# Optimization experiments

Hardware: AMD Instinct MI355X
Metric: run time of the kernel (lower is better)

Reference implementation:

```python
import jax, jax.numpy as jnp
import numpy as np

N_NODES = 100000
N_EDGES = 1600000
IN_DIM, HID_DIM, OUT_DIM = 32, 16, 8


def setup_inputs() -> dict:
    key = jax.random.key(0)
    ks = jax.random.split(key, 10)
    x = jax.random.normal(ks[0], (N_NODES, IN_DIM), dtype=jnp.float32)
    edge_index = jax.random.randint(ks[1], (2, N_EDGES), 0, N_NODES, dtype=jnp.int32)
    s1 = 1.0 / np.sqrt(IN_DIM)
    s2 = 1.0 / np.sqrt(HID_DIM)
    s3 = 1.0 / np.sqrt(OUT_DIM)
    return {
        "x": x,
        "edge_index": edge_index,
        # SAGEConv layer 1: lin_l (neighbor, with bias) and lin_r (root)
        "Wl1": jax.random.uniform(ks[2], (HID_DIM, IN_DIM), jnp.float32, -s1, s1),
        "bl1": jnp.zeros((HID_DIM,), jnp.float32),
        "Wr1": jax.random.uniform(ks[3], (HID_DIM, IN_DIM), jnp.float32, -s1, s1),
        # SAGEConv layer 2
        "Wl2": jax.random.uniform(ks[4], (OUT_DIM, HID_DIM), jnp.float32, -s2, s2),
        "bl2": jnp.zeros((OUT_DIM,), jnp.float32),
        "Wr2": jax.random.uniform(ks[5], (OUT_DIM, HID_DIM), jnp.float32, -s2, s2),
        # final Linear head
        "Wfc": jax.random.uniform(ks[6], (1, OUT_DIM), jnp.float32, -s3, s3),
        "bfc": jax.random.uniform(ks[7], (1,), jnp.float32, -s3, s3),
    }


def _sage_conv(x, src, dst, Wl, bl, Wr):
    # mean-aggregate neighbor messages x[src] at destination nodes
    msg_sum = jax.ops.segment_sum(x[src], dst, num_segments=N_NODES)  # [N, d]
    deg = jax.ops.segment_sum(jnp.ones((src.shape[0],), x.dtype), dst, num_segments=N_NODES)
    mean = msg_sum / jnp.maximum(deg, 1.0)[:, None]
    # out = lin_l(mean_neighbors) + lin_r(x_root)
    return mean @ Wl.T + bl + x @ Wr.T


def reference(x, edge_index, Wl1, bl1, Wr1, Wl2, bl2, Wr2, Wfc, bfc):
    src, dst = edge_index[0], edge_index[1]
    h = _sage_conv(x, src, dst, Wl1, bl1, Wr1)
    h = jax.nn.relu(h)
    h = _sage_conv(h, src, dst, Wl2, bl2, Wr2)
    return h @ Wfc.T + bfc  # [N, 1]
```

## Files before the change

### kernel.cpp

```cpp
#include <hip/hip_runtime.h>

#define NN 100000
#define NE 1600000
#define IN_DIM 32
#define HID_DIM 16
#define OUT_DIM 8

#define NPB 128
#define NBK ((NN + NPB - 1) / NPB)
#define CAP 3200
#define EPB 4096
#define EPT (EPB / 256)
#define NT_BUCKET ((NE + EPB - 1) / EPB)
#define NT_PRE1 ((NN + 255) / 256)
#define GRID1 (NT_BUCKET + NT_PRE1)
#define BF_STRIDE 16
#define SCAN_CHUNKS ((NBK + 255) / 256)

__global__ __launch_bounds__(256) void k_phase1(
    const float* __restrict__ x, const int* __restrict__ src, const int* __restrict__ dst,
    const float* __restrict__ Wl1, const float* __restrict__ bl1, const float* __restrict__ Wr1,
    const float* __restrict__ Wl2, const float* __restrict__ bl2, const float* __restrict__ Wr2,
    const float* __restrict__ Wfc, const float* __restrict__ bfc,
    int* __restrict__ bucketfill, unsigned int* __restrict__ bucket,
    float* __restrict__ z, float* __restrict__ rb, float* __restrict__ uvc)
{
    __shared__ int lcnt[NBK];
    __shared__ int lpos[NBK];
    __shared__ int lbase[NBK];
    __shared__ int lfill[NBK];
    __shared__ int sscan[256];
    __shared__ unsigned int ssorted[EPB];
    __shared__ unsigned short sbin[EPB];
    int tid = threadIdx.x;

    if (blockIdx.x < NT_BUCKET) {
        int e0 = blockIdx.x * EPB;
        int e1 = min(e0 + EPB, NE);
        int total = e1 - e0;

        for (int i = tid; i < NBK; i += 256) lcnt[i] = 0;
        __syncthreads();

        int myd[EPT];
#pragma unroll
        for (int k = 0; k < EPT; k++) {
            int e = e0 + k * 256 + tid;
            myd[k] = (e < e1) ? dst[e] : -1;
            if (myd[k] >= 0) atomicAdd(&lcnt[myd[k] >> 7], 1);
        }
        __syncthreads();

        int carry = 0;
        for (int ch = 0; ch < SCAN_CHUNKS; ch++) {
            int idx = ch * 256 + tid;
            int v = (idx < NBK) ? lcnt[idx] : 0;
            sscan[tid] = v;
            __syncthreads();
            for (int off = 1; off < 256; off <<= 1) {
                int t2 = (tid >= off) ? sscan[tid - off] : 0;
                __syncthreads();
                sscan[tid] += t2;
                __syncthreads();
            }
            if (idx < NBK) lpos[idx] = carry + sscan[tid] - v;
            carry += sscan[255];
            __syncthreads();
        }

        for (int i = tid; i < NBK; i += 256) {
            lbase[i] = (lcnt[i] > 0) ? atomicAdd(&bucketfill[i * BF_STRIDE], lcnt[i]) : 0;
            lfill[i] = lpos[i];
        }
        __syncthreads();

#pragma unroll
        for (int k = 0; k < EPT; k++) {
            if (myd[k] >= 0) {
                int e = e0 + k * 256 + tid;
                int s = src[e];
                int b = myd[k] >> 7;
                int p = atomicAdd(&lfill[b], 1);
                ssorted[p] = (unsigned)(myd[k] & (NPB - 1)) | ((unsigned)s << 7);
                sbin[p] = (unsigned short)b;
            }
        }
        __syncthreads();

        for (int i = tid; i < total; i += 256) {
            int b = sbin[i];
            bucket[(size_t)b * CAP + lbase[b] + (i - lpos[b])] = ssorted[i];
        }
    } else {
        int chunk = blockIdx.x - NT_BUCKET;
        float* sWl = (float*)ssorted;
        float* sWr = sWl + 512;
        float* sb  = (float*)sbin;
        for (int i = tid; i < HID_DIM * IN_DIM; i += 256) {
            sWl[i] = Wl1[i];
            sWr[i] = Wr1[i];
        }
        if (tid < HID_DIM) sb[tid] = bl1[tid];
        if (chunk == 0) {
            if (tid < HID_DIM) {
                float uu = 0.f, vv = 0.f;
#pragma unroll
                for (int o = 0; o < OUT_DIM; o++) {
                    uu += Wfc[o] * Wl2[o * HID_DIM + tid];
                    vv += Wfc[o] * Wr2[o * HID_DIM + tid];
                }
                uvc[tid] = uu;
                uvc[HID_DIM + tid] = vv;
            }
            if (tid == 0) {
                float c0 = bfc[0];
#pragma unroll
                for (int o = 0; o < OUT_DIM; o++) c0 += Wfc[o] * bl2[o];
                uvc[2 * HID_DIM] = c0;
            }
        }
        __syncthreads();
        int n = chunk * 256 + tid;
        if (n < NN) {
            float xv[IN_DIM];
            const float4* x4 = (const float4*)(x + (size_t)n * IN_DIM);
#pragma unroll
            for (int c = 0; c < 8; c++) {
                float4 b = x4[c];
                xv[c * 4 + 0] = b.x; xv[c * 4 + 1] = b.y;
                xv[c * 4 + 2] = b.z; xv[c * 4 + 3] = b.w;
            }
            float zo[HID_DIM], ro[HID_DIM];
#pragma unroll
            for (int o = 0; o < HID_DIM; o++) {
                float az = 0.f, ar = sb[o];
#pragma unroll
                for (int i = 0; i < IN_DIM; i++) {
                    az += sWl[o * IN_DIM + i] * xv[i];
                    ar += sWr[o * IN_DIM + i] * xv[i];
                }
                zo[o] = az; ro[o] = ar;
            }
            float4* z4 = (float4*)(z + (size_t)n * HID_DIM);
            float4* r4 = (float4*)(rb + (size_t)n * HID_DIM);
#pragma unroll
            for (int c = 0; c < 4; c++) {
                z4[c] = make_float4(zo[c*4], zo[c*4+1], zo[c*4+2], zo[c*4+3]);
                r4[c] = make_float4(ro[c*4], ro[c*4+1], ro[c*4+2], ro[c*4+3]);
            }
        }
    }
}

__global__ __launch_bounds__(256) void k_sort_gather(
    const int* __restrict__ bucketfill, const unsigned int* __restrict__ bucket,
    const float* __restrict__ z, const float* __restrict__ rb, const float* __restrict__ uvc,
    int* __restrict__ deg, int* __restrict__ rowstart, int* __restrict__ srcs,
    float* __restrict__ sv, float* __restrict__ tv)
{
    __shared__ int lcnt[NPB];
    __shared__ int lscan[NPB];
    __shared__ int lfill[NPB];
    __shared__ int lred[256];
    __shared__ int ssrc[CAP];

    int b = blockIdx.x;
    int tid = threadIdx.x;

    int part = 0;
    for (int i = tid; i < b; i += 256) part += bucketfill[i * BF_STRIDE];
    lred[tid] = part;
    __syncthreads();
    for (int off = 128; off > 0; off >>= 1) {
        if (tid < off) lred[tid] += lred[tid + off];
        __syncthreads();
    }
    int base = lred[0];
    int cntb = bucketfill[b * BF_STRIDE];
    const unsigned int* bk = bucket + (size_t)b * CAP;

    if (tid < NPB) lcnt[tid] = 0;
    __syncthreads();
    for (int i = tid; i < cntb; i += 256) atomicAdd(&lcnt[bk[i] & (NPB - 1)], 1);
    __syncthreads();
    if (tid < NPB) lscan[tid] = lcnt[tid];
    __syncthreads();
    for (int off = 1; off < NPB; off <<= 1) {
        int tvv = (tid >= off && tid < NPB) ? lscan[tid - off] : 0;
        __syncthreads();
        if (tid < NPB) lscan[tid] += tvv;
        __syncthreads();
    }
    if (tid < NPB) {
        int excl = lscan[tid] - lcnt[tid];
        lfill[tid] = excl;
        int node = b * NPB + tid;
        if (node < NN) { deg[node] = lcnt[tid]; rowstart[node] = base + excl; }
    }
    __syncthreads();
    for (int i = tid; i < cntb; i += 256) {
        unsigned v = bk[i];
        int d = v & (NPB - 1);
        int p = atomicAdd(&lfill[d], 1);
        int s = (int)(v >> 7);
        ssrc[p] = s;
        srcs[base + p] = s;
    }
    __syncthreads();

    int c = tid & 3;
    int nl0 = tid >> 2;
    float4 u4 = ((const float4*)uvc)[c];
    float4 v4 = ((const float4*)uvc)[4 + c];
#pragma unroll
    for (int pass = 0; pass < 2; pass++) {
        int nl = pass * 64 + nl0;
        int n2 = b * NPB + nl;
        if (n2 < NN) {
            int dg = lcnt[nl];
            int st = lscan[nl] - dg;
            float4 acc = {0.f, 0.f, 0.f, 0.f};
            for (int i = 0; i < dg; i++) {
                int sc = ssrc[st + i];
                float4 vz = ((const float4*)z)[sc * 4 + c];
                acc.x += vz.x; acc.y += vz.y; acc.z += vz.z; acc.w += vz.w;
            }
            float inv = 1.0f / fmaxf((float)dg, 1.0f);
            float4 r = ((const float4*)rb)[n2 * 4 + c];
            float h0 = fmaxf(acc.x * inv + r.x, 0.f);
            float h1 = fmaxf(acc.y * inv + r.y, 0.f);
            float h2 = fmaxf(acc.z * inv + r.z, 0.f);
            float h3 = fmaxf(acc.w * inv + r.w, 0.f);
            float ps = u4.x * h0 + u4.y * h1 + u4.z * h2 + u4.w * h3;
            float pt = v4.x * h0 + v4.y * h1 + v4.z * h2 + v4.w * h3;
            ps += __shfl_xor(ps, 1);
            ps += __shfl_xor(ps, 2);
            pt += __shfl_xor(pt, 1);
            pt += __shfl_xor(pt, 2);
            if (c == 0) { sv[n2] = ps; tv[n2] = pt; }
        }
    }
}

__global__ __launch_bounds__(256) void k_final(
    const int* __restrict__ srcs, const int* __restrict__ deg, const int* __restrict__ rowstart,
    const float* __restrict__ sv, const float* __restrict__ tv,
    const float* __restrict__ uvc, float* __restrict__ out)
{
    int v = blockIdx.x * 256 + threadIdx.x;
    if (v >= NN * 4) return;
    int n = v >> 2;
    int c = v & 3;
    int dg = deg[n];
    int st = rowstart[n];
    float acc = 0.f;
    for (int i = c; i < dg; i += 4) acc += sv[srcs[st + i]];
    acc += __shfl_xor(acc, 1);
    acc += __shfl_xor(acc, 2);
    if (c == 0) out[n] = acc / fmaxf((float)dg, 1.0f) + tv[n] + uvc[2 * HID_DIM];
}

extern "C" void kernel_launch(void* const* d_in, const int* in_sizes, int n_in,
                              void* d_out, int out_size, void* d_ws, size_t ws_size,
                              hipStream_t stream) {
    const float* x   = (const float*)d_in[0];
    const int*   ei  = (const int*)d_in[1];
    const float* Wl1 = (const float*)d_in[2];
    const float* bl1 = (const float*)d_in[3];
    const float* Wr1 = (const float*)d_in[4];
    const float* Wl2 = (const float*)d_in[5];
    const float* bl2 = (const float*)d_in[6];
    const float* Wr2 = (const float*)d_in[7];
    const float* Wfc = (const float*)d_in[8];
    const float* bfc = (const float*)d_in[9];
    float* out = (float*)d_out;

    const int* src = ei;
    const int* dst = ei + NE;

    int* bucketfill = (int*)d_ws;
    int* deg        = bucketfill + 12544;
    int* rowstart   = deg + NN;
    int* srcs       = rowstart + NN;
    float* uvc      = (float*)(srcs + NE);
    float* sv       = uvc + 40;
    float* tv       = sv + NN;
    unsigned int* bucket = (unsigned int*)(tv + NN);
    float* z        = (float*)(bucket + (size_t)NBK * CAP);
    float* rb       = z + (size_t)NN * HID_DIM;

    hipMemsetAsync(bucketfill, 0, NBK * BF_STRIDE * sizeof(int), stream);

    k_phase1<<<GRID1, 256, 0, stream>>>(x, src, dst, Wl1, bl1, Wr1,
                                        Wl2, bl2, Wr2, Wfc, bfc,
                                        bucketfill, bucket, z, rb, uvc);
    k_sort_gather<<<NBK, 256, 0, stream>>>(bucketfill, bucket, z, rb, uvc,
                                           deg, rowstart, srcs, sv, tv);
    k_final<<<((NN * 4) + 255) / 256, 256, 0, stream>>>(srcs, deg, rowstart, sv, tv, uvc, out);
}
```

Baseline: 164.5 us.

## Drop global CSR arrays; final pass re-reads buckets with LDS atomics

The sort-gather kernel no longer computes a global prefix over bucket fills or writes rowstart and the sorted source array (1.6M ints) to global memory. The final kernel now runs one block per bucket, re-reads the packed bucket entries and accumulates sv[src] into per-node shared-memory sums with LDS atomics. The layer-1 gather loop is also unrolled by four to keep more independent z loads in flight. This trades the CSR write and read traffic and the per-block serial prefix sum for a second bucket read and shared-memory float atomic contention. Float summation order also changes slightly.

```diff
diff --git a/kernel.cpp b/kernel.cpp
--- a/kernel.cpp
+++ b/kernel.cpp
@@ -155,27 +155,15 @@
 __global__ __launch_bounds__(256) void k_sort_gather(
     const int* __restrict__ bucketfill, const unsigned int* __restrict__ bucket,
     const float* __restrict__ z, const float* __restrict__ rb, const float* __restrict__ uvc,
-    int* __restrict__ deg, int* __restrict__ rowstart, int* __restrict__ srcs,
-    float* __restrict__ sv, float* __restrict__ tv)
+    int* __restrict__ deg, float* __restrict__ sv, float* __restrict__ tv)
 {
     __shared__ int lcnt[NPB];
     __shared__ int lscan[NPB];
     __shared__ int lfill[NPB];
-    __shared__ int lred[256];
     __shared__ int ssrc[CAP];
 
     int b = blockIdx.x;
     int tid = threadIdx.x;
-
-    int part = 0;
-    for (int i = tid; i < b; i += 256) part += bucketfill[i * BF_STRIDE];
-    lred[tid] = part;
-    __syncthreads();
-    for (int off = 128; off > 0; off >>= 1) {
-        if (tid < off) lred[tid] += lred[tid + off];
-        __syncthreads();
-    }
-    int base = lred[0];
     int cntb = bucketfill[b * BF_STRIDE];
     const unsigned int* bk = bucket + (size_t)b * CAP;
 
@@ -192,19 +180,16 @@
         __syncthreads();
     }
     if (tid < NPB) {
-        int excl = lscan[tid] - lcnt[tid];
-        lfill[tid] = excl;
+        lfill[tid] = lscan[tid] - lcnt[tid];
         int node = b * NPB + tid;
-        if (node < NN) { deg[node] = lcnt[tid]; rowstart[node] = base + excl; }
+        if (node < NN) deg[node] = lcnt[tid];
     }
     __syncthreads();
     for (int i = tid; i < cntb; i += 256) {
         unsigned v = bk[i];
         int d = v & (NPB - 1);
         int p = atomicAdd(&lfill[d], 1);
-        int s = (int)(v >> 7);
-        ssrc[p] = s;
-        srcs[base + p] = s;
+        ssrc[p] = (int)(v >> 7);
     }
     __syncthreads();
 
@@ -212,6 +197,7 @@
     int nl0 = tid >> 2;
     float4 u4 = ((const float4*)uvc)[c];
     float4 v4 = ((const float4*)uvc)[4 + c];
+    const float4* z4p = (const float4*)z;
 #pragma unroll
     for (int pass = 0; pass < 2; pass++) {
         int nl = pass * 64 + nl0;
@@ -220,9 +206,23 @@
             int dg = lcnt[nl];
             int st = lscan[nl] - dg;
             float4 acc = {0.f, 0.f, 0.f, 0.f};
-            for (int i = 0; i < dg; i++) {
-                int sc = ssrc[st + i];
-                float4 vz = ((const float4*)z)[sc * 4 + c];
+            int i = 0;
+            for (; i + 4 <= dg; i += 4) {
+                int s0 = ssrc[st + i + 0];
+                int s1 = ssrc[st + i + 1];
+                int s2 = ssrc[st + i + 2];
+                int s3 = ssrc[st + i + 3];
+                float4 v0 = z4p[s0 * 4 + c];
+                float4 v1 = z4p[s1 * 4 + c];
+                float4 v2 = z4p[s2 * 4 + c];
+                float4 v3 = z4p[s3 * 4 + c];
+                acc.x += v0.x + v1.x + v2.x + v3.x;
+                acc.y += v0.y + v1.y + v2.y + v3.y;
+                acc.z += v0.z + v1.z + v2.z + v3.z;
+                acc.w += v0.w + v1.w + v2.w + v3.w;
+            }
+            for (; i < dg; i++) {
+                float4 vz = z4p[ssrc[st + i] * 4 + c];
                 acc.x += vz.x; acc.y += vz.y; acc.z += vz.z; acc.w += vz.w;
             }
             float inv = 1.0f / fmaxf((float)dg, 1.0f);
@@ -243,21 +243,32 @@
 }
 
 __global__ __launch_bounds__(256) void k_final(
-    const int* __restrict__ srcs, const int* __restrict__ deg, const int* __restrict__ rowstart,
-    const float* __restrict__ sv, const float* __restrict__ tv,
+    const int* __restrict__ bucketfill, const unsigned int* __restrict__ bucket,
+    const int* __restrict__ deg, const float* __restrict__ sv, const float* __restrict__ tv,
     const float* __restrict__ uvc, float* __restrict__ out)
 {
-    int v = blockIdx.x * 256 + threadIdx.x;
-    if (v >= NN * 4) return;
-    int n = v >> 2;
-    int c = v & 3;
-    int dg = deg[n];
-    int st = rowstart[n];
-    float acc = 0.f;
-    for (int i = c; i < dg; i += 4) acc += sv[srcs[st + i]];
-    acc += __shfl_xor(acc, 1);
-    acc += __shfl_xor(acc, 2);
-    if (c == 0) out[n] = acc / fmaxf((float)dg, 1.0f) + tv[n] + uvc[2 * HID_DIM];
+    __shared__ float lsum[NPB];
+    int b = blockIdx.x;
+    int tid = threadIdx.x;
+    int cntb = bucketfill[b * BF_STRIDE];
+    const unsigned int* bk = bucket + (size_t)b * CAP;
+
+    if (tid < NPB) lsum[tid] = 0.f;
+    __syncthreads();
+    for (int i = tid; i < cntb; i += 256) {
+        unsigned v = bk[i];
+        int d = v & (NPB - 1);
+        int s = (int)(v >> 7);
+        atomicAdd(&lsum[d], sv[s]);
+    }
+    __syncthreads();
+    if (tid < NPB) {
+        int n = b * NPB + tid;
+        if (n < NN) {
+            float dg = (float)deg[n];
+            out[n] = lsum[tid] / fmaxf(dg, 1.0f) + tv[n] + uvc[2 * HID_DIM];
+        }
+    }
 }
 
 extern "C" void kernel_launch(void* const* d_in, const int* in_sizes, int n_in,
@@ -280,9 +291,7 @@
 
     int* bucketfill = (int*)d_ws;
     int* deg        = bucketfill + 12544;
-    int* rowstart   = deg + NN;
-    int* srcs       = rowstart + NN;
-    float* uvc      = (float*)(srcs + NE);
+    float* uvc      = (float*)(deg + NN);
     float* sv       = uvc + 40;
     float* tv       = sv + NN;
     unsigned int* bucket = (unsigned int*)(tv + NN);
@@ -294,7 +303,6 @@
     k_phase1<<<GRID1, 256, 0, stream>>>(x, src, dst, Wl1, bl1, Wr1,
                                         Wl2, bl2, Wr2, Wfc, bfc,
                                         bucketfill, bucket, z, rb, uvc);
-    k_sort_gather<<<NBK, 256, 0, stream>>>(bucketfill, bucket, z, rb, uvc,
-                                           deg, rowstart, srcs, sv, tv);
-    k_final<<<((NN * 4) + 255) / 256, 256, 0, stream>>>(srcs, deg, rowstart, sv, tv, uvc, out);
+    k_sort_gather<<<NBK, 256, 0, stream>>>(bucketfill, bucket, z, rb, uvc, deg, sv, tv);
+    k_final<<<NBK, 256, 0, stream>>>(bucketfill, bucket, deg, sv, tv, uvc, out);
 }
```

After: 159.2 us. 1.03x faster.
